# Kernel optimization log

Hardware: AMD Instinct MI355X
Metric: run time of the kernel (lower is better)

The kernel has to match this reference:

```python
import jax, jax.numpy as jnp
import numpy as np

B, S, F, H = 64, 1024, 128, 512  # batch, seq_len, features, lstm units


def setup_inputs() -> dict:
    key = jax.random.key(0)
    k1, k2, k3 = jax.random.split(key, 3)
    x = jax.random.normal(k1, (B, S, F), dtype=jnp.float32)
    # Keras LSTM params: kernel [F, 4H], recurrent_kernel [H, 4H], bias [4H]
    W = jax.random.normal(k2, (F, 4 * H), dtype=jnp.float32) * (1.0 / np.sqrt(F))
    U = jax.random.normal(k3, (H, 4 * H), dtype=jnp.float32) * (1.0 / np.sqrt(H))
    b = jnp.zeros((4 * H,), dtype=jnp.float32)
    return {"x": x, "W": W, "U": U, "b": b}


def _lstm_relu(x, W, U, b):
    # Precompute input projection for all timesteps: [B,S,4H]
    xW = jnp.einsum("bsf,fg->bsg", x, W) + b
    xW_t = jnp.transpose(xW, (1, 0, 2))  # [S,B,4H] for scan over time
    h0 = jnp.zeros((x.shape[0], H), dtype=x.dtype)
    c0 = jnp.zeros((x.shape[0], H), dtype=x.dtype)

    def step(carry, xw):
        h, c = carry
        z = xw + h @ U  # [B,4H]
        zi, zf, zg, zo = jnp.split(z, 4, axis=-1)  # Keras gate order i,f,c,o
        i = jax.nn.sigmoid(zi)
        f = jax.nn.sigmoid(zf)
        g = jax.nn.relu(zg)          # activation='relu' (candidate)
        o = jax.nn.sigmoid(zo)
        c_new = f * c + i * g
        h_new = o * jax.nn.relu(c_new)  # activation='relu' (output)
        return (h_new, c_new), h_new

    _, hs = jax.lax.scan(step, (h0, c0), xW_t)
    return jnp.transpose(hs, (1, 0, 2))  # [B,S,H]


def reference(x, W, U, b):
    # LSTM(return_sequences=True, activation='relu'); Dropout inactive at inference.
    return _lstm_relu(x, W, U, b)
```

## Files before the change

kernel.cpp:

```cpp
#include <hip/hip_runtime.h>
#include <stdint.h>


#define S_ 1024
#define F_ 128
#define H_ 512
#define G4_ 2048
#define KH 16
#define KDIM 640
#define LDKS 648
#define HB (64 * H_)

typedef __attribute__((ext_vector_type(8))) short short8;
typedef __attribute__((ext_vector_type(4))) float f32x4;
typedef unsigned long long ull;

__device__ __forceinline__ unsigned short f2bf(float f) {
  union { float f; unsigned u; } v; v.f = f;
  unsigned u = v.u + 0x7fffu + ((v.u >> 16) & 1u);
  return (unsigned short)(u >> 16);
}

__device__ __forceinline__ short8 pack2(f32x4 a, f32x4 b) {
  short8 r;
#pragma unroll
  for (int i = 0; i < 4; ++i) r[i] = (short)f2bf(a[i]);
#pragma unroll
  for (int i = 0; i < 4; ++i) r[4 + i] = (short)f2bf(b[i]);
  return r;
}

__global__ __launch_bounds__(256, 1) void lstm_pers(
    const float* __restrict__ x, const float* __restrict__ W,
    const float* __restrict__ U, const float* __restrict__ bias,
    float* __restrict__ out, unsigned int* ws_sync, unsigned short* hbuf) {

  __shared__ unsigned short V[64 * LDKS];
  __shared__ f32x4 R[4][4][64];
  __shared__ int meta[2];
  __shared__ unsigned join_ctr;

  const int tid  = threadIdx.x;
  const int w    = tid >> 6;
  const int lane = tid & 63;
  const int l15  = lane & 15;
  const int l4   = lane >> 4;
  const int koff = l4 * 8;

  if (tid == 0) {
    unsigned int xcc;
    asm volatile("s_getreg_b32 %0, hwreg(20, 0, 4)" : "=s"(xcc));
    xcc &= 7;
    unsigned sv = atomicAdd(ws_sync + xcc * 32, 1u);
    meta[0] = (int)xcc;
    meta[1] = (int)(sv & 31);
    join_ctr = 0u;
  }
  __syncthreads();
  const int xcc  = meta[0];
  const int slot = meta[1];

  unsigned int* gline  = ws_sync + 256 + xcc * 32;
  unsigned int* myflag = gline + slot;
  unsigned int* pollp  = gline + (lane & 31);

  const int u0    = slot * 16;
  const int bbase = xcc * 8;

  for (int idx = tid; idx < (64 * KDIM) / 4; idx += 256) {
    const int q4   = idx & 15;
    const int k    = idx >> 4;
    const int gate = q4 & 3;
    const int ul0  = (q4 >> 2) * 4;
    const int col  = gate * H_ + u0 + ul0;
    const float* src = (k < H_) ? (U + (size_t)k * G4_ + col)
                                : (W + (size_t)(k - H_) * G4_ + col);
    const f32x4 v4 = *(const f32x4*)src;
#pragma unroll
    for (int q = 0; q < 4; ++q) {
      const int ul = ul0 + q;
      const int cc = (ul >> 2) * 16 + (ul & 3) * 4 + gate;
      V[cc * LDKS + k] = f2bf(v4[q]);
    }
  }

  float bias_r[4];
#pragma unroll
  for (int g = 0; g < 4; ++g) bias_r[g] = bias[g * H_ + u0 + w * 4 + l4];

  __syncthreads();

  const int brow = bbase + (l15 & 7);
  const float* xrow = x + (size_t)brow * S_ * F_ + koff + w * 32;
  const unsigned short* hrow0 = hbuf + (size_t)brow * H_ + koff;
  const int myunit = u0 + w * 4 + l4;

  float cst = 0.f;

  f32x4 xa = *(const f32x4*)(xrow);
  f32x4 xb = *(const f32x4*)(xrow + 4);

  for (int t = 0; t < S_; ++t) {
    f32x4 acc[4];
#pragma unroll
    for (int tl = 0; tl < 4; ++tl) { acc[tl][0]=0.f; acc[tl][1]=0.f; acc[tl][2]=0.f; acc[tl][3]=0.f; }
    {
      const short8 bx = pack2(xa, xb);
      const int k0 = (KH + w) * 32 + koff;
#pragma unroll
      for (int tl = 0; tl < 4; ++tl) {
        const short8 a = *(const short8*)&V[(tl * 16 + l15) * LDKS + k0];
        acc[tl] = __builtin_amdgcn_mfma_f32_16x16x32_bf16(a, bx, acc[tl], 0, 0, 0);
      }
    }

    {
      const int tn = (t + 1 < S_) ? t + 1 : t;
      const float* xt = xrow + (size_t)tn * F_;
      xa = *(const f32x4*)(xt);
      xb = *(const f32x4*)(xt + 4);
    }

    if (t > 0 && w == 0) {
      const unsigned tgt = (unsigned)t;
      while (true) {
        const unsigned v = __hip_atomic_load(pollp, __ATOMIC_RELAXED, __HIP_MEMORY_SCOPE_AGENT);
        if (__all((int)(v >= tgt))) break;
        __builtin_amdgcn_s_sleep(1);
      }
    }
    __syncthreads();

    if (t > 0) {
      const unsigned short* hr = hrow0 + (size_t)(t & 1) * HB;
      short8 bh[4];
#pragma unroll
      for (int i = 0; i < 4; ++i) {
        union { ull u[2]; short8 s; } bb;
        const ull* hq = (const ull*)(hr + (4 * w + i) * 32);
        bb.u[0] = __hip_atomic_load(hq,     __ATOMIC_RELAXED, __HIP_MEMORY_SCOPE_AGENT);
        bb.u[1] = __hip_atomic_load(hq + 1, __ATOMIC_RELAXED, __HIP_MEMORY_SCOPE_AGENT);
        bh[i] = bb.s;
      }
#pragma unroll
      for (int i = 0; i < 4; ++i) {
        const int k0 = (4 * w + i) * 32 + koff;
#pragma unroll
        for (int tl = 0; tl < 4; ++tl) {
          const short8 a = *(const short8*)&V[(tl * 16 + l15) * LDKS + k0];
          acc[tl] = __builtin_amdgcn_mfma_f32_16x16x32_bf16(a, bh[i], acc[tl], 0, 0, 0);
        }
      }
    }

#pragma unroll
    for (int tl = 0; tl < 4; ++tl) R[w][tl][lane] = acc[tl];
    __syncthreads();

    f32x4 z;
    {
      const f32x4 r0 = R[0][w][lane], r1 = R[1][w][lane],
                  r2 = R[2][w][lane], r3 = R[3][w][lane];
#pragma unroll
      for (int g = 0; g < 4; ++g)
        z[g] = bias_r[g] + r0[g] + r1[g] + r2[g] + r3[g];
    }

    const float ig = 1.f / (1.f + __expf(-z[0]));
    const float fg = 1.f / (1.f + __expf(-z[1]));
    const float gg = fmaxf(z[2], 0.f);
    const float og = 1.f / (1.f + __expf(-z[3]));
    const float cn = fg * cst + ig * gg;
    cst = cn;
    const float hv = og * fmaxf(cn, 0.f);

    if (l15 < 8)
      hbuf[(size_t)((t + 1) & 1) * HB + (size_t)brow * H_ + myunit] = f2bf(hv);
    asm volatile("s_waitcnt vmcnt(0)" ::: "memory");

    if (lane == 0) {
      const unsigned old = atomicAdd(&join_ctr, 1u);
      if (old == 4u * (unsigned)t + 3u)
        __hip_atomic_store(myflag, (unsigned)(t + 1),
                           __ATOMIC_RELAXED, __HIP_MEMORY_SCOPE_AGENT);
    }

    if (l15 < 8)
      out[((size_t)brow * S_ + t) * H_ + myunit] = hv;
  }
}

extern "C" void kernel_launch(void* const* d_in, const int* in_sizes, int n_in,
                              void* d_out, int out_size, void* d_ws, size_t ws_size,
                              hipStream_t stream) {
  const float* x = (const float*)d_in[0];
  const float* W = (const float*)d_in[1];
  const float* U = (const float*)d_in[2];
  const float* b = (const float*)d_in[3];
  float* out = (float*)d_out;

  unsigned int*   ws_sync = (unsigned int*)d_ws;
  unsigned short* hbuf    = (unsigned short*)((char*)d_ws + 32768);

  hipMemsetAsync(d_ws, 0, 32768, stream);

  lstm_pers<<<dim3(256), dim3(256), 0, stream>>>(x, W, U, b, out, ws_sync, hbuf);
}
```

Measured before the change: 2.791 ms.

## Replace flag barrier with sign-bit tagged h exchange and pairwise wave reduction

Drops the per-step global flag poll and block-wide barriers. Each h value now carries a parity tag in its bf16 sign bit, so consumers spin directly on the hidden-state data until every tag matches, and the tag is masked off before the MFMA. Work is re-split so each wave pair covers half of K for two tiles and exchanges partial sums through LDS flags instead of a 4-way reduction behind __syncthreads. An epoch counter guards buffer reuse two steps back. The risk is subtle memory-ordering bugs and reliance on ReLU outputs being non-negative so the sign bit is free; the memset also grows to clear hbuf.

```diff
diff --git a/kernel.cpp b/kernel.cpp
--- a/kernel.cpp
+++ b/kernel.cpp
@@ -10,6 +10,8 @@
 #define KDIM 640
 #define LDKS 648
 #define HB (64 * H_)
+#define SMASK8 0x8000800080008000ull
+#define VMASK8 0x7FFF7FFF7FFF7FFFull
 
 typedef __attribute__((ext_vector_type(8))) short short8;
 typedef __attribute__((ext_vector_type(4))) float f32x4;
@@ -36,9 +38,10 @@
     float* __restrict__ out, unsigned int* ws_sync, unsigned short* hbuf) {
 
   __shared__ unsigned short V[64 * LDKS];
-  __shared__ f32x4 R[4][4][64];
+  __shared__ f32x4 Rx[2][4][64];
+  __shared__ unsigned lflag[4];
+  __shared__ unsigned jctr;
   __shared__ int meta[2];
-  __shared__ unsigned join_ctr;
 
   const int tid  = threadIdx.x;
   const int w    = tid >> 6;
@@ -54,15 +57,16 @@
     unsigned sv = atomicAdd(ws_sync + xcc * 32, 1u);
     meta[0] = (int)xcc;
     meta[1] = (int)(sv & 31);
-    join_ctr = 0u;
+    jctr = 0u;
   }
+  if (tid < 4) lflag[tid] = 0u;
   __syncthreads();
   const int xcc  = meta[0];
   const int slot = meta[1];
 
-  unsigned int* gline  = ws_sync + 256 + xcc * 32;
-  unsigned int* myflag = gline + slot;
-  unsigned int* pollp  = gline + (lane & 31);
+  unsigned int* eline = ws_sync + 256 + xcc * 32;
+  unsigned int* myep  = eline + slot;
+  unsigned int* epp   = eline + (lane & 31);
 
   const int u0    = slot * 16;
   const int bbase = xcc * 8;
@@ -90,99 +94,129 @@
 
   __syncthreads();
 
-  const int brow = bbase + (l15 & 7);
-  const float* xrow = x + (size_t)brow * S_ * F_ + koff + w * 32;
-  const unsigned short* hrow0 = hbuf + (size_t)brow * H_ + koff;
+  const int brow   = bbase + (l15 & 7);
   const int myunit = u0 + w * 4 + l4;
+  const int tA     = (w >> 1) * 2;
+  const int khb    = (w & 1) * 8;
+  const int own    = w & 1;
+
+  const float* xrow = x + (size_t)brow * S_ * F_ + (w & 1) * 64 + koff;
+  const unsigned short* hrowc = hbuf + (size_t)brow * H_ + koff;
 
   float cst = 0.f;
 
-  f32x4 xa = *(const f32x4*)(xrow);
-  f32x4 xb = *(const f32x4*)(xrow + 4);
+  f32x4 xq0 = *(const f32x4*)(xrow);
+  f32x4 xq1 = *(const f32x4*)(xrow + 4);
+  f32x4 xq2 = *(const f32x4*)(xrow + 32);
+  f32x4 xq3 = *(const f32x4*)(xrow + 36);
 
   for (int t = 0; t < S_; ++t) {
-    f32x4 acc[4];
-#pragma unroll
-    for (int tl = 0; tl < 4; ++tl) { acc[tl][0]=0.f; acc[tl][1]=0.f; acc[tl][2]=0.f; acc[tl][3]=0.f; }
+    unsigned ev = 0xFFFFFFFFu;
+    if (t >= 2)
+      ev = __hip_atomic_load(epp, __ATOMIC_RELAXED, __HIP_MEMORY_SCOPE_AGENT);
+
+    f32x4 acc0 = {0.f, 0.f, 0.f, 0.f};
+    f32x4 acc1 = {0.f, 0.f, 0.f, 0.f};
     {
-      const short8 bx = pack2(xa, xb);
-      const int k0 = (KH + w) * 32 + koff;
-#pragma unroll
-      for (int tl = 0; tl < 4; ++tl) {
-        const short8 a = *(const short8*)&V[(tl * 16 + l15) * LDKS + k0];
-        acc[tl] = __builtin_amdgcn_mfma_f32_16x16x32_bf16(a, bx, acc[tl], 0, 0, 0);
-      }
+      const short8 bx0 = pack2(xq0, xq1);
+      const short8 bx1 = pack2(xq2, xq3);
+      const int k0a = (KH + (w & 1) * 2) * 32 + koff;
+      const int k0b = k0a + 32;
+      const short8 aA0 = *(const short8*)&V[(tA * 16 + l15) * LDKS + k0a];
+      const short8 aB0 = *(const short8*)&V[((tA + 1) * 16 + l15) * LDKS + k0a];
+      const short8 aA1 = *(const short8*)&V[(tA * 16 + l15) * LDKS + k0b];
+      const short8 aB1 = *(const short8*)&V[((tA + 1) * 16 + l15) * LDKS + k0b];
+      acc0 = __builtin_amdgcn_mfma_f32_16x16x32_bf16(aA0, bx0, acc0, 0, 0, 0);
+      acc1 = __builtin_amdgcn_mfma_f32_16x16x32_bf16(aB0, bx0, acc1, 0, 0, 0);
+      acc0 = __builtin_amdgcn_mfma_f32_16x16x32_bf16(aA1, bx1, acc0, 0, 0, 0);
+      acc1 = __builtin_amdgcn_mfma_f32_16x16x32_bf16(aB1, bx1, acc1, 0, 0, 0);
     }
 
     {
       const int tn = (t + 1 < S_) ? t + 1 : t;
       const float* xt = xrow + (size_t)tn * F_;
-      xa = *(const f32x4*)(xt);
-      xb = *(const f32x4*)(xt + 4);
-    }
-
-    if (t > 0 && w == 0) {
-      const unsigned tgt = (unsigned)t;
+      xq0 = *(const f32x4*)(xt);
+      xq1 = *(const f32x4*)(xt + 4);
+      xq2 = *(const f32x4*)(xt + 32);
+      xq3 = *(const f32x4*)(xt + 36);
+    }
+
+    if (t > 0) {
+      const ull tm = (((((unsigned)(t - 1)) >> 1) & 1u) ^ 1u) ? SMASK8 : 0ull;
+      const unsigned short* hr = hrowc + (size_t)(t & 1) * HB;
+      ull hv_[16];
       while (true) {
-        const unsigned v = __hip_atomic_load(pollp, __ATOMIC_RELAXED, __HIP_MEMORY_SCOPE_AGENT);
-        if (__all((int)(v >= tgt))) break;
-        __builtin_amdgcn_s_sleep(1);
+#pragma unroll
+        for (int i = 0; i < 8; ++i) {
+          const ull* q = (const ull*)(hr + (khb + i) * 32);
+          hv_[2 * i]     = __hip_atomic_load(q,     __ATOMIC_RELAXED, __HIP_MEMORY_SCOPE_AGENT);
+          hv_[2 * i + 1] = __hip_atomic_load(q + 1, __ATOMIC_RELAXED, __HIP_MEMORY_SCOPE_AGENT);
+        }
+        ull orx = 0;
+#pragma unroll
+        for (int i = 0; i < 16; ++i) orx |= (hv_[i] ^ tm);
+        if (__all((int)((orx & 0x8000ull) == 0)))
+          break;
       }
-    }
-    __syncthreads();
-
-    if (t > 0) {
-      const unsigned short* hr = hrow0 + (size_t)(t & 1) * HB;
-      short8 bh[4];
-#pragma unroll
-      for (int i = 0; i < 4; ++i) {
+#pragma unroll
+      for (int i = 0; i < 8; ++i) {
         union { ull u[2]; short8 s; } bb;
-        const ull* hq = (const ull*)(hr + (4 * w + i) * 32);
-        bb.u[0] = __hip_atomic_load(hq,     __ATOMIC_RELAXED, __HIP_MEMORY_SCOPE_AGENT);
-        bb.u[1] = __hip_atomic_load(hq + 1, __ATOMIC_RELAXED, __HIP_MEMORY_SCOPE_AGENT);
-        bh[i] = bb.s;
+        bb.u[0] = hv_[2 * i] & VMASK8;
+        bb.u[1] = hv_[2 * i + 1] & VMASK8;
+        const int k0 = (khb + i) * 32 + koff;
+        const short8 aA = *(const short8*)&V[(tA * 16 + l15) * LDKS + k0];
+        const short8 aB = *(const short8*)&V[((tA + 1) * 16 + l15) * LDKS + k0];
+        acc0 = __builtin_amdgcn_mfma_f32_16x16x32_bf16(aA, bb.s, acc0, 0, 0, 0);
+        acc1 = __builtin_amdgcn_mfma_f32_16x16x32_bf16(aB, bb.s, acc1, 0, 0, 0);
       }
-#pragma unroll
-      for (int i = 0; i < 4; ++i) {
-        const int k0 = (4 * w + i) * 32 + koff;
-#pragma unroll
-        for (int tl = 0; tl < 4; ++tl) {
-          const short8 a = *(const short8*)&V[(tl * 16 + l15) * LDKS + k0];
-          acc[tl] = __builtin_amdgcn_mfma_f32_16x16x32_bf16(a, bh[i], acc[tl], 0, 0, 0);
-        }
-      }
-    }
-
-#pragma unroll
-    for (int tl = 0; tl < 4; ++tl) R[w][tl][lane] = acc[tl];
-    __syncthreads();
-
-    f32x4 z;
-    {
-      const f32x4 r0 = R[0][w][lane], r1 = R[1][w][lane],
-                  r2 = R[2][w][lane], r3 = R[3][w][lane];
-#pragma unroll
-      for (int g = 0; g < 4; ++g)
-        z[g] = bias_r[g] + r0[g] + r1[g] + r2[g] + r3[g];
-    }
-
-    const float ig = 1.f / (1.f + __expf(-z[0]));
-    const float fg = 1.f / (1.f + __expf(-z[1]));
-    const float gg = fmaxf(z[2], 0.f);
-    const float og = 1.f / (1.f + __expf(-z[3]));
+    }
+
+    if (lane == 0) {
+      const unsigned old = atomicAdd(&jctr, 1u);
+      if (old == 4u * (unsigned)t + 3u)
+        __hip_atomic_store(myep, (unsigned)t, __ATOMIC_RELAXED, __HIP_MEMORY_SCOPE_AGENT);
+    }
+
+    const f32x4 accO = own ? acc1 : acc0;
+    const f32x4 accP = own ? acc0 : acc1;
+    const int p = t & 1;
+    Rx[p][w ^ 1][lane] = accP;
+    __hip_atomic_store(&lflag[w], (unsigned)(t + 1),
+                       __ATOMIC_RELEASE, __HIP_MEMORY_SCOPE_WORKGROUP);
+    while (__hip_atomic_load(&lflag[w ^ 1], __ATOMIC_ACQUIRE,
+                             __HIP_MEMORY_SCOPE_WORKGROUP) < (unsigned)(t + 1)) {}
+    const f32x4 pp = Rx[p][w][lane];
+
+    const float z0 = bias_r[0] + accO[0] + pp[0];
+    const float z1 = bias_r[1] + accO[1] + pp[1];
+    const float z2 = bias_r[2] + accO[2] + pp[2];
+    const float z3 = bias_r[3] + accO[3] + pp[3];
+    const float ig = 1.f / (1.f + __expf(-z0));
+    const float fg = 1.f / (1.f + __expf(-z1));
+    const float gg = fmaxf(z2, 0.f);
+    const float og = 1.f / (1.f + __expf(-z3));
     const float cn = fg * cst + ig * gg;
     cst = cn;
     const float hv = og * fmaxf(cn, 0.f);
 
-    if (l15 < 8)
-      hbuf[(size_t)((t + 1) & 1) * HB + (size_t)brow * H_ + myunit] = f2bf(hv);
-    asm volatile("s_waitcnt vmcnt(0)" ::: "memory");
-
-    if (lane == 0) {
-      const unsigned old = atomicAdd(&join_ctr, 1u);
-      if (old == 4u * (unsigned)t + 3u)
-        __hip_atomic_store(myflag, (unsigned)(t + 1),
-                           __ATOMIC_RELAXED, __HIP_MEMORY_SCOPE_AGENT);
+    const unsigned hb0 = (unsigned)f2bf(hv);
+    const unsigned hb1 = (unsigned)__shfl((int)hb0, (lane & 7) + 16);
+    const unsigned hb2 = (unsigned)__shfl((int)hb0, (lane & 7) + 32);
+    const unsigned hb3 = (unsigned)__shfl((int)hb0, (lane & 7) + 48);
+    const ull tagw = (((((unsigned)t) >> 1) & 1u) ^ 1u) ? SMASK8 : 0ull;
+    const ull wrd = (ull)(hb0 & 0xFFFFu) | ((ull)(hb1 & 0xFFFFu) << 16) |
+                    ((ull)(hb2 & 0xFFFFu) << 32) | ((ull)(hb3 & 0xFFFFu) << 48) | tagw;
+
+    if (t >= 2) {
+      const unsigned tgt = (unsigned)(t - 1);
+      while (!__all((int)(ev >= tgt)))
+        ev = __hip_atomic_load(epp, __ATOMIC_RELAXED, __HIP_MEMORY_SCOPE_AGENT);
+    }
+
+    if (lane < 8) {
+      ull* dst = (ull*)(hbuf + (size_t)((t + 1) & 1) * HB +
+                        (size_t)(bbase + lane) * H_ + u0 + w * 4);
+      __hip_atomic_store(dst, wrd, __ATOMIC_RELAXED, __HIP_MEMORY_SCOPE_AGENT);
     }
 
     if (l15 < 8)
@@ -202,7 +236,7 @@
   unsigned int*   ws_sync = (unsigned int*)d_ws;
   unsigned short* hbuf    = (unsigned short*)((char*)d_ws + 32768);
 
-  hipMemsetAsync(d_ws, 0, 32768, stream);
+  hipMemsetAsync(d_ws, 0, 32768 + 2 * HB * sizeof(unsigned short), stream);
 
   lstm_pers<<<dim3(256), dim3(256), 0, stream>>>(x, W, U, b, out, ws_sync, hbuf);
 }
```

Measured after the change: 10.36 ms. 3.71x slower.
